# Kernel tuning notes

Measured on AMD Instinct MI355X. Metric: run time of the kernel, lower is better.

## Reference

```python
import jax, jax.numpy as jnp
import numpy as np


def setup_inputs() -> dict:
    key = jax.random.key(0)
    k1, k2, k3 = jax.random.split(key, 3)
    B, C, H, W = 8, 256, 64, 64
    x = jax.random.normal(k1, (B, C, H, W), dtype=jnp.float32)
    mask = (jax.random.uniform(k2, (B, 1, H, W)) < 0.5).astype(jnp.float32)
    # Conv1d(2C, C, kernel_size=1) == matmul with weight (C, 2C) + bias (C,)
    Wc = jax.random.normal(k3, (C, 2 * C), dtype=jnp.float32) * 0.02
    bc = jnp.zeros((C,), dtype=jnp.float32)
    return {"x": x, "mask": mask, "Wc": Wc, "bc": bc}


def reference(x, mask, Wc, bc):
    B, C, H, W = x.shape
    N = H * W
    EPS = 1e-8
    # mask.detach() + nearest interpolate to x's spatial size (sizes already match)
    m = jax.lax.stop_gradient(mask)
    q = (x * m).reshape(B, C, N)              # masked (foreground) features
    s = (x * (1.0 - m)).reshape(B, C, N)      # support (background) features
    q = q / (jnp.linalg.norm(q, axis=1, keepdims=True) + EPS)
    s = s / (jnp.linalg.norm(s, axis=1, keepdims=True) + EPS)
    # per-batch cosine similarity: (B, N, N)
    sim = jnp.einsum('bcn,bcm->bnm', q, s)
    # top-1 over support dim (k = 1)
    idx = jnp.argmax(sim, axis=2)             # (B, N) selected support index per query pos
    wv = jnp.max(sim, axis=2)                 # (B, N) top-1 similarity value
    fore_wv = jnp.max(sim, axis=1)            # (B, N) top-1 over query dim
    fm = m.reshape(B, N)
    # faithful quirk: validmask = validmask[0, :, 0] keeps only support position 0 -> per-sample scalar
    valid = ((fore_wv[:, 0] > 0.5).astype(x.dtype) * fm[:, 0])[:, None, None]  # (B,1,1)
    # gather selected support features: select[b,c,j] = s[b,c,idx[b,j]]
    select = jnp.take_along_axis(s, idx[:, None, :], axis=2)  # (B, C, N)
    # faithful quirk: with k=1, Softmax(dim=-1) acts over the H*W axis (same per channel)
    w = jax.nn.softmax(wv, axis=-1)           # (B, N)
    fuse = select * w[:, None, :]             # (B, C, N)  (sum over k=1 is identity)
    hybrid = jnp.concatenate([fuse, q], axis=1)               # (B, 2C, N)
    hybrid = jnp.einsum('bin,oi->bon', hybrid, Wc) + bc[None, :, None]  # 1x1 conv
    hybrid = hybrid * valid + q * (1.0 - valid)
    refined = hybrid.reshape(B, C, H, W)
    # attmask holds only the LAST sample's indices (loop variable overwritten)
    attmap = jnp.zeros((B, N), dtype=x.dtype).at[:, idx[-1]].set(1.0)
    attmap = attmap.reshape(B, 1, H, W)
    attmap = jnp.repeat(jnp.repeat(attmap, 8, axis=2), 8, axis=3)  # nearest x8 upsample
    out = refined * m + x * (1.0 - m)
    return out, attmap
```

## Files before the change

kernel.cpp:

```cpp
#include <hip/hip_runtime.h>
#include <cmath>

#define B_ 8
#define C_ 256
#define N_ 4096
#define EPS_ 1e-8f

typedef _Float16 half8 __attribute__((ext_vector_type(8)));
typedef float f32x4 __attribute__((ext_vector_type(4)));
typedef unsigned short ushort8 __attribute__((ext_vector_type(8)));

__device__ __forceinline__ void gload_lds16(const void* g, void* l) {
  __builtin_amdgcn_global_load_lds((const __attribute__((address_space(1))) unsigned int*)g,
                                   (__attribute__((address_space(3))) unsigned int*)l, 16, 0, 0);
}

__device__ __forceinline__ float block_fore(const float* __restrict__ partMax, int b) {
  int l = threadIdx.x & 63;
  float v = partMax[(b << 6) + l];
#pragma unroll
  for (int d = 32; d; d >>= 1) v = fmaxf(v, __shfl_xor(v, d, 64));
  return v;
}

__global__ __launch_bounds__(512) void k_base(const float* __restrict__ x, const float* __restrict__ mask,
                                              float* __restrict__ fq, float* __restrict__ fs,
                                              float* __restrict__ out, float* __restrict__ partMax,
                                              int* __restrict__ mark,
                                              unsigned short* __restrict__ qhi, unsigned short* __restrict__ qlo,
                                              unsigned short* __restrict__ shi, unsigned short* __restrict__ slo,
                                              int* __restrict__ rowsrc, int* __restrict__ rowrank,
                                              int* __restrict__ colsrc, int* __restrict__ colmapG,
                                              int* __restrict__ cnt) {
  int b = blockIdx.y, n0 = blockIdx.x << 6;
  int t = threadIdx.x;
  if (b == B_) {
    if (blockIdx.x != 0) return;
    __shared__ int wtot[8], wbase[8], stot_s;
    int n0c = t << 3;
#pragma unroll
    for (int i = 0; i < 8; ++i) {
      rowsrc[t + (i << 9)] = 0;
      colsrc[t + (i << 9)] = 0;
      colmapG[t + (i << 9)] = 0x3fffffff;
    }
    __syncthreads();
    int f[8]; int pk = 0;
#pragma unroll
    for (int i = 0; i < 8; ++i) {
      int m = (mask[(7 << 12) + n0c + i] != 0.f) ? 1 : 0;
      f[i] = m;
      pk += m ? 1 : (1 << 16);
    }
    int incl = pk;
#pragma unroll
    for (int d = 1; d < 64; d <<= 1) {
      int o = __shfl_up(incl, d, 64);
      if ((t & 63) >= d) incl += o;
    }
    if ((t & 63) == 63) wtot[t >> 6] = incl;
    __syncthreads();
    if (t < 8) {
      int s2 = 0;
      for (int i = 0; i < t; ++i) s2 += wtot[i];
      wbase[t] = s2;
      if (t == 7) stot_s = s2 + wtot[7];
    }
    __syncthreads();
    int excl = wbase[t >> 6] + incl - pk;
    int rslot = excl & 0xffff, cslot = excl >> 16;
#pragma unroll
    for (int i = 0; i < 8; ++i) {
      int n2 = n0c + i;
      if (f[i]) { rowsrc[rslot] = n2; rowrank[n2] = rslot; ++rslot; }
      else      { rowrank[n2] = -1; colsrc[cslot] = n2; colmapG[cslot] = n2; ++cslot; }
    }
    __syncthreads();
    if (t == 0) {
      int tot = stot_s;
      int nr = tot & 0xffff;
      cnt[0] = nr;
      cnt[1] = tot >> 16;
      cnt[2] = (nr > 0) ? rowsrc[0] : 0x7fffffff;
    }
    return;
  }
  int ln = t & 63, cg = t >> 6;
  __shared__ float sred[512];
  __shared__ float s0[256];
  __shared__ float rss[8][64], rdp[8][64];
  __shared__ float scaleS[64], f64q[64], f64s[64];
  __shared__ float bcast[2];
  if (b == 0 && blockIdx.x == 0) {
#pragma unroll
    for (int i = 0; i < 8; ++i) mark[t + (i << 9)] = 0;
  }
  const size_t xbase = ((size_t)b * C_) << 12;
  float xc0 = 0.f;
  if (t < 256) xc0 = x[xbase + ((size_t)t << 12)];
  sred[t] = xc0 * xc0;
  __syncthreads();
  for (int s = 256; s; s >>= 1) { if (t < s) sred[t] += sred[t + s]; __syncthreads(); }
  if (t == 0) { bcast[0] = 1.f / (sqrtf(sred[0]) + EPS_); bcast[1] = mask[b << 12]; }
  __syncthreads();
  if (t < 256) s0[t] = xc0 * ((1.f - bcast[1]) * bcast[0]);
  __syncthreads();
  int n = n0 + ln;
  const float* xp = x + xbase + (((size_t)cg) << 17) + n;
  float xv[32];
  float ss = 0.f, dp = 0.f;
#pragma unroll
  for (int c = 0; c < 32; ++c) {
    float v = xp[(size_t)c << 12];
    xv[c] = v;
    ss += v * v;
    dp += v * s0[(cg << 5) + c];
  }
  rss[cg][ln] = ss; rdp[cg][ln] = dp;
  __syncthreads();
  if (t < 64) {
    float sst = 0.f, dpt = 0.f;
#pragma unroll
    for (int g = 0; g < 8; ++g) { sst += rss[g][t]; dpt += rdp[g][t]; }
    float inv = 1.f / (sqrtf(sst) + EPS_);
    float m = mask[(b << 12) + n0 + t];
    float fqv = m * inv;
    fq[(b << 12) + n0 + t] = fqv;
    fs[(b << 12) + n0 + t] = (1.f - m) * inv;
    scaleS[t] = (m != 0.f) ? inv : 1.f;
    f64q[t] = fqv * 64.0f;
    f64s[t] = (1.f - m) * inv * 64.0f;
    float val = dpt * fqv;
#pragma unroll
    for (int d = 32; d; d >>= 1) val = fmaxf(val, __shfl_xor(val, d, 64));
    if (t == 0) partMax[(b << 6) + blockIdx.x] = val;
  }
  __syncthreads();
  float sc = scaleS[ln];
  float* op = out + xbase + (((size_t)cg) << 17) + n;
#pragma unroll
  for (int c = 0; c < 32; ++c) op[(size_t)c << 12] = xv[c] * sc;
  if (b == B_ - 1) {
    float fqn = f64q[ln], fsn = f64s[ln];
    size_t rowbase = ((size_t)n) << 8;
#pragma unroll
    for (int j = 0; j < 4; ++j) {
      ushort8 vqh, vql, vsh, vsl;
#pragma unroll
      for (int i = 0; i < 8; ++i) {
        float xvv = xv[j * 8 + i];
        float qv = xvv * fqn;
        _Float16 qh = (_Float16)qv;
        _Float16 ql = (_Float16)((qv - (float)qh) * 2048.0f);
        float sv = xvv * fsn;
        _Float16 sh = (_Float16)sv;
        _Float16 sl = (_Float16)((sv - (float)sh) * 2048.0f);
        vqh[i] = __builtin_bit_cast(unsigned short, qh);
        vql[i] = __builtin_bit_cast(unsigned short, ql);
        vsh[i] = __builtin_bit_cast(unsigned short, sh);
        vsl[i] = __builtin_bit_cast(unsigned short, sl);
      }
      size_t off = rowbase + ((size_t)cg << 5) + ((size_t)j << 3);
      *reinterpret_cast<ushort8*>(qhi + off) = vqh;
      *reinterpret_cast<ushort8*>(qlo + off) = vql;
      *reinterpret_cast<ushort8*>(shi + off) = vsh;
      *reinterpret_cast<ushort8*>(slo + off) = vsl;
    }
  }
}

__global__ __launch_bounds__(256, 2) void k_sim7(const unsigned short* __restrict__ qhi, const unsigned short* __restrict__ qlo,
                                                 const unsigned short* __restrict__ shi, const unsigned short* __restrict__ slo,
                                                 const int* __restrict__ rowsrc, const int* __restrict__ colsrc,
                                                 const int* __restrict__ colmapG, const int* __restrict__ cnt,
                                                 float* __restrict__ partV, int* __restrict__ partI) {
  int nrows = cnt[0], ncols = cnt[1];
  int bid = blockIdx.x;
  int mt = bid & 31, nt = bid >> 5;
  if ((nt << 7) >= nrows || (mt << 7) >= ncols) return;
  int tid = threadIdx.x;
  int w = tid >> 6, lane = tid & 63;
  int wy = w >> 1, wx = w & 1;
  __shared__ __align__(16) unsigned short smem[2][16384];

  f32x4 acc_h[4][4], acc_c[4][4];
#pragma unroll
  for (int i = 0; i < 4; ++i)
#pragma unroll
    for (int j = 0; j < 4; ++j) {
      acc_h[i][j] = (f32x4){0.f, 0.f, 0.f, 0.f};
      acc_c[i][j] = (f32x4){0.f, 0.f, 0.f, 0.f};
    }

  const unsigned short* gsrc = (w == 0) ? qhi : (w == 1) ? qlo : (w == 2) ? shi : slo;
  const int* srcmap = (w < 2) ? rowsrc : colsrc;
  int n0 = ((w < 2) ? nt : mt) << 7;
  int lrow = lane >> 2, lch = lane & 3;
  int chx = (lch ^ ((lrow >> 1) & 3)) << 3;
  int s = lane >> 4, c16 = lane & 15;
  int srco[8];
#pragma unroll
  for (int seg = 0; seg < 8; ++seg)
    srco[seg] = (srcmap[n0 + (seg << 4) + lrow] << 8) + chx;

#define STAGE7(buf, kt)                                                                \
  _Pragma("unroll")                                                                    \
  for (int seg = 0; seg < 8; ++seg) {                                                  \
    const unsigned short* g = gsrc + (size_t)(srco[seg] + ((kt) << 5));                \
    gload_lds16(g, &smem[buf][(w << 12) + (seg << 9)]);                                \
  }

  STAGE7(0, 0);

  int cur = 0;
  for (int kt = 0; kt < 8; ++kt) {
    if (kt < 7) {
      STAGE7(cur ^ 1, kt + 1);
      asm volatile("s_waitcnt vmcnt(8)" ::: "memory");
    } else {
      asm volatile("s_waitcnt vmcnt(0)" ::: "memory");
    }
    __builtin_amdgcn_s_barrier();
    __builtin_amdgcn_sched_barrier(0);
    const unsigned short* sm = &smem[cur][0];
    half8 ah[4], al[4], bh[4], bl[4];
#pragma unroll
    for (int f = 0; f < 4; ++f) {
      int ra = (wy << 6) + (f << 4) + c16;
      int oa = ra * 32 + ((s ^ ((ra >> 1) & 3)) << 3);
      ah[f] = *reinterpret_cast<const half8*>(&sm[oa]);
      al[f] = *reinterpret_cast<const half8*>(&sm[4096 + oa]);
      int rb = (wx << 6) + (f << 4) + c16;
      int ob = rb * 32 + ((s ^ ((rb >> 1) & 3)) << 3);
      bh[f] = *reinterpret_cast<const half8*>(&sm[8192 + ob]);
      bl[f] = *reinterpret_cast<const half8*>(&sm[12288 + ob]);
    }
#pragma unroll
    for (int fi = 0; fi < 4; ++fi)
#pragma unroll
      for (int fj = 0; fj < 4; ++fj) {
        acc_h[fi][fj] = __builtin_amdgcn_mfma_f32_16x16x32_f16(ah[fi], bh[fj], acc_h[fi][fj], 0, 0, 0);
        acc_c[fi][fj] = __builtin_amdgcn_mfma_f32_16x16x32_f16(ah[fi], bl[fj], acc_c[fi][fj], 0, 0, 0);
        acc_c[fi][fj] = __builtin_amdgcn_mfma_f32_16x16x32_f16(al[fi], bh[fj], acc_c[fi][fj], 0, 0, 0);
      }
    asm volatile("s_waitcnt lgkmcnt(0)" ::: "memory");
    __builtin_amdgcn_s_barrier();
    __builtin_amdgcn_sched_barrier(0);
    cur ^= 1;
  }
#undef STAGE7
  int cg4[4], cok[4];
#pragma unroll
  for (int fj = 0; fj < 4; ++fj) {
    int slotg = (mt << 7) + (wx << 6) + (fj << 4) + c16;
    cg4[fj] = colmapG[slotg];
    cok[fj] = slotg < ncols;
  }
  float* redV = reinterpret_cast<float*>(&smem[0][0]);
  int* redI = reinterpret_cast<int*>(&smem[0][512]);
  int g16 = lane >> 4;
#pragma unroll
  for (int fi = 0; fi < 4; ++fi)
#pragma unroll
    for (int r2 = 0; r2 < 4; ++r2) {
      float bv = -INFINITY; int bi = 0x7fffffff;
#pragma unroll
      for (int fj = 0; fj < 4; ++fj) {
        float v = cok[fj] ? (acc_h[fi][fj][r2] + acc_c[fi][fj][r2] * (1.0f / 2048.0f)) * (1.0f / 4096.0f)
                          : -INFINITY;
        int colg = cg4[fj];
        if (v > bv) { bv = v; bi = colg; }
      }
#pragma unroll
      for (int d = 1; d < 16; d <<= 1) {
        float ov = __shfl_xor(bv, d, 64);
        int oi = __shfl_xor(bi, d, 64);
        if (ov > bv || (ov == bv && oi < bi)) { bv = ov; bi = oi; }
      }
      if (c16 == 0) {
        int row = (wy << 6) + (fi << 4) + (g16 << 2) + r2;
        redV[row * 2 + wx] = bv;
        redI[row * 2 + wx] = bi;
      }
    }
  __syncthreads();
  if (tid < 128) {
    float v0 = redV[tid * 2], v1 = redV[tid * 2 + 1];
    int i0 = redI[tid * 2], i1 = redI[tid * 2 + 1];
    if (v1 > v0 || (v1 == v0 && i1 < i0)) { v0 = v1; i0 = i1; }
    int n = (nt << 7) + tid;
    partV[(((size_t)n) << 5) + mt] = v0;
    partI[(((size_t)n) << 5) + mt] = i0;
  }
}

__global__ __launch_bounds__(256) void k_mid(const float* __restrict__ x, const float* __restrict__ mask,
                                             const float* __restrict__ partMax,
                                             const float* __restrict__ fq, const float* __restrict__ fs,
                                             const float* __restrict__ p7V, const int* __restrict__ p7I,
                                             const int* __restrict__ rowrank, const int* __restrict__ cnt,
                                             float* __restrict__ wv, int* __restrict__ idxv,
                                             int* __restrict__ mark) {
  int bid = blockIdx.x;
  int tid = threadIdx.x;
  if (bid < 16) {
    int n = bid * 256 + tid;
    int ncols = cnt[1], j0 = cnt[2];
    int rk = rowrank[n];
    float bv; int bi;
    if (rk < 0) {
      bv = 0.f; bi = 0;
    } else {
      bv = -INFINITY; bi = 0x7fffffff;
      int mtmax = (ncols + 127) >> 7;
      for (int mt = 0; mt < mtmax; ++mt) {
        float v = p7V[(((size_t)rk) << 5) + mt];
        int i = p7I[(((size_t)rk) << 5) + mt];
        if (v > bv || (v == bv && i < bi)) { bv = v; bi = i; }
      }
      if (j0 < N_) {
        if (0.f > bv) { bv = 0.f; bi = j0; }
        else if (0.f == bv && j0 < bi) bi = j0;
      }
    }
    wv[((B_ - 1) << 12) + n] = bv;
    idxv[((B_ - 1) << 12) + n] = bi;
    mark[bi] = 1;
    return;
  }
  int rr = bid - 16;
  int b = rr >> 6;
  float fore = block_fore(partMax, b);
  if (!(fore > 0.5f) || mask[b << 12] == 0.f) return;
  int n0 = (rr & 63) << 6;
  int tx = tid & 15, ty = tid >> 4;
  int lk = ty, ln4 = tx << 2;

  __shared__ float As[16][68];
  __shared__ float Bs[16][68];
  __shared__ float fqs[64], fss[64];
  __shared__ float rv[64][17];
  __shared__ int ri[64][17];

  if (tid < 64) fqs[tid] = fq[(b << 12) + n0 + tid];

  float bestv[4]; int besti[4];
#pragma unroll
  for (int i = 0; i < 4; ++i) { bestv[i] = -INFINITY; besti[i] = 0; }

  const size_t xb = ((size_t)b * C_) << 12;

  for (int m0 = 0; m0 < N_; m0 += 64) {
    if (tid < 64) fss[tid] = fs[(b << 12) + m0 + tid];
    float cacc[4][4];
#pragma unroll
    for (int i = 0; i < 4; ++i)
#pragma unroll
      for (int j = 0; j < 4; ++j) cacc[i][j] = 0.f;
    __syncthreads();
    for (int kt = 0; kt < C_; kt += 16) {
      float4 va = *reinterpret_cast<const float4*>(x + xb + ((size_t)(kt + lk) << 12) + n0 + ln4);
      float4 vb = *reinterpret_cast<const float4*>(x + xb + ((size_t)(kt + lk) << 12) + m0 + ln4);
      va.x *= fqs[ln4]; va.y *= fqs[ln4 + 1]; va.z *= fqs[ln4 + 2]; va.w *= fqs[ln4 + 3];
      vb.x *= fss[ln4]; vb.y *= fss[ln4 + 1]; vb.z *= fss[ln4 + 2]; vb.w *= fss[ln4 + 3];
      *reinterpret_cast<float4*>(&As[lk][ln4]) = va;
      *reinterpret_cast<float4*>(&Bs[lk][ln4]) = vb;
      __syncthreads();
#pragma unroll
      for (int k = 0; k < 16; ++k) {
        float a0 = As[k][(ty << 2) + 0], a1 = As[k][(ty << 2) + 1], a2 = As[k][(ty << 2) + 2], a3 = As[k][(ty << 2) + 3];
        float b0 = Bs[k][(tx << 2) + 0], b1 = Bs[k][(tx << 2) + 1], b2 = Bs[k][(tx << 2) + 2], b3 = Bs[k][(tx << 2) + 3];
        cacc[0][0] += a0 * b0; cacc[0][1] += a0 * b1; cacc[0][2] += a0 * b2; cacc[0][3] += a0 * b3;
        cacc[1][0] += a1 * b0; cacc[1][1] += a1 * b1; cacc[1][2] += a1 * b2; cacc[1][3] += a1 * b3;
        cacc[2][0] += a2 * b0; cacc[2][1] += a2 * b1; cacc[2][2] += a2 * b2; cacc[2][3] += a2 * b3;
        cacc[3][0] += a3 * b0; cacc[3][1] += a3 * b1; cacc[3][2] += a3 * b2; cacc[3][3] += a3 * b3;
      }
      __syncthreads();
    }
#pragma unroll
    for (int j = 0; j < 4; ++j) {
      int col = m0 + (tx << 2) + j;
#pragma unroll
      for (int i = 0; i < 4; ++i) {
        float v = cacc[i][j];
        if (v > bestv[i]) { bestv[i] = v; besti[i] = col; }
      }
    }
  }
#pragma unroll
  for (int i = 0; i < 4; ++i) { rv[(ty << 2) + i][tx] = bestv[i]; ri[(ty << 2) + i][tx] = besti[i]; }
  __syncthreads();
  if (tid < 64) {
    float bv = rv[tid][0]; int bi = ri[tid][0];
#pragma unroll
    for (int t2 = 1; t2 < 16; ++t2) {
      float v = rv[tid][t2]; int ii = ri[tid][t2];
      if (v > bv || (v == bv && ii < bi)) { bv = v; bi = ii; }
    }
    wv[(b << 12) + n0 + tid] = bv;
    idxv[(b << 12) + n0 + tid] = bi;
  }
}

__global__ __launch_bounds__(256) void k_epi(const int* __restrict__ mark, float* __restrict__ att,
                                             const float* __restrict__ x, const float* __restrict__ mask,
                                             const float* __restrict__ partMax,
                                             const float* __restrict__ fq, const float* __restrict__ fs,
                                             const float* __restrict__ Wc, const float* __restrict__ bc,
                                             const int* __restrict__ idxv, const float* __restrict__ wv,
                                             float* __restrict__ out) {
  int bid = blockIdx.x;
  int tid = threadIdx.x;
  if (bid < 1024) {
    int id = bid * 256 + tid;
    int x8 = (id & 63) << 3;
    int y = (id >> 6) & 511;
    int b = id >> 15;
    float v = mark[((y >> 3) << 6) + (x8 >> 3)] ? 1.f : 0.f;
    float4 vv = make_float4(v, v, v, v);
    float* p = att + (((size_t)b) << 18) + (y << 9) + x8;
    *reinterpret_cast<float4*>(p) = vv;
    *reinterpret_cast<float4*>(p + 4) = vv;
    return;
  }
  int rr = bid - 1024;
  int b = rr >> 4;
  int bx = rr & 15;
  float fore = block_fore(partMax, b);
  if (!(fore > 0.5f) || mask[b << 12] == 0.f) return;
  __shared__ float red[256];
  float mx = -INFINITY;
  for (int n = tid; n < N_; n += 256) mx = fmaxf(mx, wv[(b << 12) + n]);
  red[tid] = mx; __syncthreads();
  for (int s = 128; s; s >>= 1) { if (tid < s) red[tid] = fmaxf(red[tid], red[tid + s]); __syncthreads(); }
  mx = red[0]; __syncthreads();
  float sm = 0.f;
  for (int n = tid; n < N_; n += 256) sm += expf(wv[(b << 12) + n] - mx);
  red[tid] = sm; __syncthreads();
  for (int s = 128; s; s >>= 1) { if (tid < s) red[tid] += red[tid + s]; __syncthreads(); }
  float den = red[0];

  int n = bx * 256 + tid;
  int bn = (b << 12) + n;
  float mn = mask[bn];
  if (mn == 0.f) return;
  int j = idxv[bn];
  float w = expf(wv[bn] - mx) / den;
  float fsj = fs[(b << 12) + j];
  float fqn = fq[bn];
  const float* xb = x + (((size_t)b * C_) << 12);
  for (int o = 0; o < C_; ++o) {
    const float* wr = Wc + o * 2 * C_;
    float a1 = 0.f, a2 = 0.f;
    for (int i = 0; i < C_; ++i) {
      a1 += wr[i] * xb[((size_t)i << 12) + j];
      a2 += wr[C_ + i] * xb[((size_t)i << 12) + n];
    }
    out[((size_t)(b * C_ + o) << 12) + n] = bc[o] + a1 * (fsj * w) + a2 * fqn;
  }
}

extern "C" void kernel_launch(void* const* d_in, const int* in_sizes, int n_in,
                              void* d_out, int out_size, void* d_ws, size_t ws_size,
                              hipStream_t stream) {
  const float* x = (const float*)d_in[0];
  const float* mask = (const float*)d_in[1];
  const float* Wc = (const float*)d_in[2];
  const float* bc = (const float*)d_in[3];
  float* out = (float*)d_out;
  float* att = out + (size_t)B_ * C_ * N_;

  float* wsf = (float*)d_ws;
  float* fq = wsf;
  float* fs = wsf + 32768;
  float* wv = wsf + 65536;
  int* idxv = (int*)(wsf + 98304);
  int* rowsrc = (int*)(wsf + 131072);
  int* rowrank = (int*)(wsf + 135168);
  int* colsrc = (int*)(wsf + 139264);
  int* colmapG = (int*)(wsf + 143360);
  int* cnt = (int*)(wsf + 147456);
  int* mark = (int*)(wsf + 655392);
  float* partMax = wsf + 659488;
  float* p7V = wsf + 660000;
  int* p7I = (int*)(wsf + 791072);
  unsigned short* qhi = (unsigned short*)(wsf + 922144);
  unsigned short* qlo = (unsigned short*)(wsf + 1446432);
  unsigned short* shi = (unsigned short*)(wsf + 1970720);
  unsigned short* slo = (unsigned short*)(wsf + 2495008);

  k_base<<<dim3(64, B_ + 1), 512, 0, stream>>>(x, mask, fq, fs, out, partMax, mark,
                                               qhi, qlo, shi, slo,
                                               rowsrc, rowrank, colsrc, colmapG, cnt);
  k_sim7<<<1024, 256, 0, stream>>>(qhi, qlo, shi, slo, rowsrc, colsrc, colmapG, cnt, p7V, p7I);
  k_mid<<<464, 256, 0, stream>>>(x, mask, partMax, fq, fs, p7V, p7I, rowrank, cnt, wv, idxv, mark);
  k_epi<<<1152, 256, 0, stream>>>(mark, att, x, mask, partMax, fq, fs, Wc, bc, idxv, wv, out);
}
```

Baseline: 62.40 us.

## Fuse sim7 and mid kernels with last-block atomic reduction and 8-wave tiles

```diff
diff --git a/kernel.cpp b/kernel.cpp
--- a/kernel.cpp
+++ b/kernel.cpp
@@ -82,6 +82,7 @@
       cnt[0] = nr;
       cnt[1] = tot >> 16;
       cnt[2] = (nr > 0) ? rowsrc[0] : 0x7fffffff;
+      cnt[4] = 0;
     }
     return;
   }
@@ -169,178 +170,200 @@
   }
 }
 
-__global__ __launch_bounds__(256, 2) void k_sim7(const unsigned short* __restrict__ qhi, const unsigned short* __restrict__ qlo,
+__global__ __launch_bounds__(512, 2) void k_sim7(const unsigned short* __restrict__ qhi, const unsigned short* __restrict__ qlo,
                                                  const unsigned short* __restrict__ shi, const unsigned short* __restrict__ slo,
-                                                 const int* __restrict__ rowsrc, const int* __restrict__ colsrc,
-                                                 const int* __restrict__ colmapG, const int* __restrict__ cnt,
-                                                 float* __restrict__ partV, int* __restrict__ partI) {
-  int nrows = cnt[0], ncols = cnt[1];
-  int bid = blockIdx.x;
-  int mt = bid & 31, nt = bid >> 5;
-  if ((nt << 7) >= nrows || (mt << 7) >= ncols) return;
-  int tid = threadIdx.x;
-  int w = tid >> 6, lane = tid & 63;
-  int wy = w >> 1, wx = w & 1;
+                                                 const int* __restrict__ rowsrc, const int* __restrict__ rowrank,
+                                                 const int* __restrict__ colsrc, const int* __restrict__ colmapG,
+                                                 int* __restrict__ cnt,
+                                                 float* __restrict__ partV, int* __restrict__ partI,
+                                                 const float* __restrict__ x, const float* __restrict__ mask,
+                                                 const float* __restrict__ partMax,
+                                                 const float* __restrict__ fq, const float* __restrict__ fs,
+                                                 float* __restrict__ wv, int* __restrict__ idxv,
+                                                 int* __restrict__ mark) {
   __shared__ __align__(16) unsigned short smem[2][16384];
-
-  f32x4 acc_h[4][4], acc_c[4][4];
-#pragma unroll
-  for (int i = 0; i < 4; ++i)
-#pragma unroll
-    for (int j = 0; j < 4; ++j) {
-      acc_h[i][j] = (f32x4){0.f, 0.f, 0.f, 0.f};
-      acc_c[i][j] = (f32x4){0.f, 0.f, 0.f, 0.f};
-    }
-
-  const unsigned short* gsrc = (w == 0) ? qhi : (w == 1) ? qlo : (w == 2) ? shi : slo;
-  const int* srcmap = (w < 2) ? rowsrc : colsrc;
-  int n0 = ((w < 2) ? nt : mt) << 7;
-  int lrow = lane >> 2, lch = lane & 3;
-  int chx = (lch ^ ((lrow >> 1) & 3)) << 3;
-  int s = lane >> 4, c16 = lane & 15;
-  int srco[8];
-#pragma unroll
-  for (int seg = 0; seg < 8; ++seg)
-    srco[seg] = (srcmap[n0 + (seg << 4) + lrow] << 8) + chx;
-
-#define STAGE7(buf, kt)                                                                \
-  _Pragma("unroll")                                                                    \
-  for (int seg = 0; seg < 8; ++seg) {                                                  \
-    const unsigned short* g = gsrc + (size_t)(srco[seg] + ((kt) << 5));                \
-    gload_lds16(g, &smem[buf][(w << 12) + (seg << 9)]);                                \
-  }
-
-  STAGE7(0, 0);
-
-  int cur = 0;
-  for (int kt = 0; kt < 8; ++kt) {
-    if (kt < 7) {
-      STAGE7(cur ^ 1, kt + 1);
-      asm volatile("s_waitcnt vmcnt(8)" ::: "memory");
-    } else {
-      asm volatile("s_waitcnt vmcnt(0)" ::: "memory");
-    }
-    __builtin_amdgcn_s_barrier();
-    __builtin_amdgcn_sched_barrier(0);
-    const unsigned short* sm = &smem[cur][0];
-    half8 ah[4], al[4], bh[4], bl[4];
-#pragma unroll
-    for (int f = 0; f < 4; ++f) {
-      int ra = (wy << 6) + (f << 4) + c16;
-      int oa = ra * 32 + ((s ^ ((ra >> 1) & 3)) << 3);
-      ah[f] = *reinterpret_cast<const half8*>(&sm[oa]);
-      al[f] = *reinterpret_cast<const half8*>(&sm[4096 + oa]);
-      int rb = (wx << 6) + (f << 4) + c16;
-      int ob = rb * 32 + ((s ^ ((rb >> 1) & 3)) << 3);
-      bh[f] = *reinterpret_cast<const half8*>(&sm[8192 + ob]);
-      bl[f] = *reinterpret_cast<const half8*>(&sm[12288 + ob]);
-    }
-#pragma unroll
-    for (int fi = 0; fi < 4; ++fi)
-#pragma unroll
-      for (int fj = 0; fj < 4; ++fj) {
-        acc_h[fi][fj] = __builtin_amdgcn_mfma_f32_16x16x32_f16(ah[fi], bh[fj], acc_h[fi][fj], 0, 0, 0);
-        acc_c[fi][fj] = __builtin_amdgcn_mfma_f32_16x16x32_f16(ah[fi], bl[fj], acc_c[fi][fj], 0, 0, 0);
-        acc_c[fi][fj] = __builtin_amdgcn_mfma_f32_16x16x32_f16(al[fi], bh[fj], acc_c[fi][fj], 0, 0, 0);
-      }
-    asm volatile("s_waitcnt lgkmcnt(0)" ::: "memory");
-    __builtin_amdgcn_s_barrier();
-    __builtin_amdgcn_sched_barrier(0);
-    cur ^= 1;
-  }
-#undef STAGE7
-  int cg4[4], cok[4];
-#pragma unroll
-  for (int fj = 0; fj < 4; ++fj) {
-    int slotg = (mt << 7) + (wx << 6) + (fj << 4) + c16;
-    cg4[fj] = colmapG[slotg];
-    cok[fj] = slotg < ncols;
-  }
-  float* redV = reinterpret_cast<float*>(&smem[0][0]);
-  int* redI = reinterpret_cast<int*>(&smem[0][512]);
-  int g16 = lane >> 4;
-#pragma unroll
-  for (int fi = 0; fi < 4; ++fi)
-#pragma unroll
-    for (int r2 = 0; r2 < 4; ++r2) {
-      float bv = -INFINITY; int bi = 0x7fffffff;
-#pragma unroll
-      for (int fj = 0; fj < 4; ++fj) {
-        float v = cok[fj] ? (acc_h[fi][fj][r2] + acc_c[fi][fj][r2] * (1.0f / 2048.0f)) * (1.0f / 4096.0f)
-                          : -INFINITY;
-        int colg = cg4[fj];
-        if (v > bv) { bv = v; bi = colg; }
-      }
-#pragma unroll
-      for (int d = 1; d < 16; d <<= 1) {
-        float ov = __shfl_xor(bv, d, 64);
-        int oi = __shfl_xor(bi, d, 64);
-        if (ov > bv || (ov == bv && oi < bi)) { bv = ov; bi = oi; }
-      }
-      if (c16 == 0) {
-        int row = (wy << 6) + (fi << 4) + (g16 << 2) + r2;
-        redV[row * 2 + wx] = bv;
-        redI[row * 2 + wx] = bi;
-      }
-    }
-  __syncthreads();
-  if (tid < 128) {
-    float v0 = redV[tid * 2], v1 = redV[tid * 2 + 1];
-    int i0 = redI[tid * 2], i1 = redI[tid * 2 + 1];
-    if (v1 > v0 || (v1 == v0 && i1 < i0)) { v0 = v1; i0 = i1; }
-    int n = (nt << 7) + tid;
-    partV[(((size_t)n) << 5) + mt] = v0;
-    partI[(((size_t)n) << 5) + mt] = i0;
-  }
-}
-
-__global__ __launch_bounds__(256) void k_mid(const float* __restrict__ x, const float* __restrict__ mask,
-                                             const float* __restrict__ partMax,
-                                             const float* __restrict__ fq, const float* __restrict__ fs,
-                                             const float* __restrict__ p7V, const int* __restrict__ p7I,
-                                             const int* __restrict__ rowrank, const int* __restrict__ cnt,
-                                             float* __restrict__ wv, int* __restrict__ idxv,
-                                             int* __restrict__ mark) {
+  __shared__ int lastblk;
   int bid = blockIdx.x;
   int tid = threadIdx.x;
-  if (bid < 16) {
-    int n = bid * 256 + tid;
-    int ncols = cnt[1], j0 = cnt[2];
-    int rk = rowrank[n];
-    float bv; int bi;
-    if (rk < 0) {
-      bv = 0.f; bi = 0;
-    } else {
-      bv = -INFINITY; bi = 0x7fffffff;
-      int mtmax = (ncols + 127) >> 7;
-      for (int mt = 0; mt < mtmax; ++mt) {
-        float v = p7V[(((size_t)rk) << 5) + mt];
-        int i = p7I[(((size_t)rk) << 5) + mt];
-        if (v > bv || (v == bv && i < bi)) { bv = v; bi = i; }
-      }
-      if (j0 < N_) {
-        if (0.f > bv) { bv = 0.f; bi = j0; }
-        else if (0.f == bv && j0 < bi) bi = j0;
-      }
-    }
-    wv[((B_ - 1) << 12) + n] = bv;
-    idxv[((B_ - 1) << 12) + n] = bi;
-    mark[bi] = 1;
+
+  if (bid < 1024) {
+    int nrows = cnt[0], ncols = cnt[1];
+    int mt = bid & 31, nt = bid >> 5;
+    int active = !(((nt << 7) >= nrows) || ((mt << 7) >= ncols));
+    if (active) {
+      int w = tid >> 6, lane = tid & 63;
+      int wy = w >> 2, wx = w & 3;
+      int arr = w >> 1, shalf = w & 1;
+
+      f32x4 acc_h[4][2], acc_c[4][2];
+#pragma unroll
+      for (int i = 0; i < 4; ++i)
+#pragma unroll
+        for (int j = 0; j < 2; ++j) {
+          acc_h[i][j] = (f32x4){0.f, 0.f, 0.f, 0.f};
+          acc_c[i][j] = (f32x4){0.f, 0.f, 0.f, 0.f};
+        }
+
+      const unsigned short* gsrc = (arr == 0) ? qhi : (arr == 1) ? qlo : (arr == 2) ? shi : slo;
+      const int* srcmap = (arr < 2) ? rowsrc : colsrc;
+      int n0 = ((arr < 2) ? nt : mt) << 7;
+      int lrow = lane >> 2, lch = lane & 3;
+      int chx = (lch ^ ((lrow >> 1) & 3)) << 3;
+      int s = lane >> 4, c16 = lane & 15;
+      int srco[4];
+#pragma unroll
+      for (int s2 = 0; s2 < 4; ++s2) {
+        int seg = (shalf << 2) + s2;
+        srco[s2] = (srcmap[n0 + (seg << 4) + lrow] << 8) + chx;
+      }
+
+#define STAGE7(buf, kt)                                                                   \
+  _Pragma("unroll")                                                                       \
+  for (int s2 = 0; s2 < 4; ++s2) {                                                        \
+    const unsigned short* g = gsrc + (size_t)(srco[s2] + ((kt) << 5));                    \
+    gload_lds16(g, &smem[buf][(arr << 12) + ((((shalf << 2) + s2)) << 9)]);               \
+  }
+
+      STAGE7(0, 0);
+
+      int cur = 0;
+      for (int kt = 0; kt < 8; ++kt) {
+        if (kt < 7) {
+          STAGE7(cur ^ 1, kt + 1);
+          asm volatile("s_waitcnt vmcnt(4)" ::: "memory");
+        } else {
+          asm volatile("s_waitcnt vmcnt(0)" ::: "memory");
+        }
+        __builtin_amdgcn_s_barrier();
+        __builtin_amdgcn_sched_barrier(0);
+        const unsigned short* sm = &smem[cur][0];
+        half8 ah[4], al[4], bh[2], bl[2];
+#pragma unroll
+        for (int f = 0; f < 4; ++f) {
+          int ra = (wy << 6) + (f << 4) + c16;
+          int oa = ra * 32 + ((s ^ ((ra >> 1) & 3)) << 3);
+          ah[f] = *reinterpret_cast<const half8*>(&sm[oa]);
+          al[f] = *reinterpret_cast<const half8*>(&sm[4096 + oa]);
+        }
+#pragma unroll
+        for (int f = 0; f < 2; ++f) {
+          int rb = (wx << 5) + (f << 4) + c16;
+          int ob = rb * 32 + ((s ^ ((rb >> 1) & 3)) << 3);
+          bh[f] = *reinterpret_cast<const half8*>(&sm[8192 + ob]);
+          bl[f] = *reinterpret_cast<const half8*>(&sm[12288 + ob]);
+        }
+#pragma unroll
+        for (int fi = 0; fi < 4; ++fi)
+#pragma unroll
+          for (int fj = 0; fj < 2; ++fj) {
+            acc_h[fi][fj] = __builtin_amdgcn_mfma_f32_16x16x32_f16(ah[fi], bh[fj], acc_h[fi][fj], 0, 0, 0);
+            acc_c[fi][fj] = __builtin_amdgcn_mfma_f32_16x16x32_f16(ah[fi], bl[fj], acc_c[fi][fj], 0, 0, 0);
+            acc_c[fi][fj] = __builtin_amdgcn_mfma_f32_16x16x32_f16(al[fi], bh[fj], acc_c[fi][fj], 0, 0, 0);
+          }
+        asm volatile("s_waitcnt lgkmcnt(0)" ::: "memory");
+        __builtin_amdgcn_s_barrier();
+        __builtin_amdgcn_sched_barrier(0);
+        cur ^= 1;
+      }
+#undef STAGE7
+      int cg4[2], cok[2];
+#pragma unroll
+      for (int fj = 0; fj < 2; ++fj) {
+        int slotg = (mt << 7) + (wx << 5) + (fj << 4) + c16;
+        cg4[fj] = colmapG[slotg];
+        cok[fj] = slotg < ncols;
+      }
+      float* redV = reinterpret_cast<float*>(&smem[0][0]);
+      int* redI = reinterpret_cast<int*>(&smem[0][1024]);
+      int g16 = lane >> 4;
+#pragma unroll
+      for (int fi = 0; fi < 4; ++fi)
+#pragma unroll
+        for (int r2 = 0; r2 < 4; ++r2) {
+          float bv = -INFINITY; int bi = 0x7fffffff;
+#pragma unroll
+          for (int fj = 0; fj < 2; ++fj) {
+            float v = cok[fj] ? (acc_h[fi][fj][r2] + acc_c[fi][fj][r2] * (1.0f / 2048.0f)) * (1.0f / 4096.0f)
+                              : -INFINITY;
+            int colg = cg4[fj];
+            if (v > bv) { bv = v; bi = colg; }
+          }
+#pragma unroll
+          for (int d = 1; d < 16; d <<= 1) {
+            float ov = __shfl_xor(bv, d, 64);
+            int oi = __shfl_xor(bi, d, 64);
+            if (ov > bv || (ov == bv && oi < bi)) { bv = ov; bi = oi; }
+          }
+          if (c16 == 0) {
+            int row = (wy << 6) + (fi << 4) + (g16 << 2) + r2;
+            redV[row * 4 + wx] = bv;
+            redI[row * 4 + wx] = bi;
+          }
+        }
+      __syncthreads();
+      if (tid < 128) {
+        float bv = redV[tid * 4]; int bi = redI[tid * 4];
+#pragma unroll
+        for (int q = 1; q < 4; ++q) {
+          float v = redV[tid * 4 + q]; int i = redI[tid * 4 + q];
+          if (v > bv || (v == bv && i < bi)) { bv = v; bi = i; }
+        }
+        int n = (nt << 7) + tid;
+        partV[(((size_t)n) << 5) + mt] = bv;
+        partI[(((size_t)n) << 5) + mt] = bi;
+      }
+    }
+    __threadfence();
+    if (tid == 0) {
+      int old = atomicAdd(&cnt[4], 1);
+      lastblk = (old == 1023) ? 1 : 0;
+    }
+    __syncthreads();
+    if (lastblk) {
+      __threadfence();
+      int ncols2 = cnt[1], j0 = cnt[2];
+      int mtmax = (ncols2 + 127) >> 7;
+#pragma unroll
+      for (int rr2 = 0; rr2 < 8; ++rr2) {
+        int n = (rr2 << 9) + tid;
+        int rk = rowrank[n];
+        float bv; int bi;
+        if (rk < 0) {
+          bv = 0.f; bi = 0;
+        } else {
+          bv = -INFINITY; bi = 0x7fffffff;
+          for (int mt2 = 0; mt2 < mtmax; ++mt2) {
+            float v = partV[(((size_t)rk) << 5) + mt2];
+            int i = partI[(((size_t)rk) << 5) + mt2];
+            if (v > bv || (v == bv && i < bi)) { bv = v; bi = i; }
+          }
+          if (j0 < N_) {
+            if (0.f > bv) { bv = 0.f; bi = j0; }
+            else if (0.f == bv && j0 < bi) bi = j0;
+          }
+        }
+        wv[((B_ - 1) << 12) + n] = bv;
+        idxv[((B_ - 1) << 12) + n] = bi;
+        mark[bi] = 1;
+      }
+    }
     return;
   }
-  int rr = bid - 16;
+
+  int rr = bid - 1024;
   int b = rr >> 6;
   float fore = block_fore(partMax, b);
   if (!(fore > 0.5f) || mask[b << 12] == 0.f) return;
+  if (tid >= 256) return;
   int n0 = (rr & 63) << 6;
   int tx = tid & 15, ty = tid >> 4;
   int lk = ty, ln4 = tx << 2;
-
-  __shared__ float As[16][68];
-  __shared__ float Bs[16][68];
-  __shared__ float fqs[64], fss[64];
-  __shared__ float rv[64][17];
-  __shared__ int ri[64][17];
+  float* As = reinterpret_cast<float*>(&smem[0][0]);
+  float* Bs = As + 1088;
+  float* fqs = Bs + 1088;
+  float* fss = fqs + 64;
+  float* rv = fss + 64;
+  int* ri = reinterpret_cast<int*>(rv + 1088);
 
   if (tid < 64) fqs[tid] = fq[(b << 12) + n0 + tid];
 
@@ -363,13 +386,15 @@
       float4 vb = *reinterpret_cast<const float4*>(x + xb + ((size_t)(kt + lk) << 12) + m0 + ln4);
       va.x *= fqs[ln4]; va.y *= fqs[ln4 + 1]; va.z *= fqs[ln4 + 2]; va.w *= fqs[ln4 + 3];
       vb.x *= fss[ln4]; vb.y *= fss[ln4 + 1]; vb.z *= fss[ln4 + 2]; vb.w *= fss[ln4 + 3];
-      *reinterpret_cast<float4*>(&As[lk][ln4]) = va;
-      *reinterpret_cast<float4*>(&Bs[lk][ln4]) = vb;
+      *reinterpret_cast<float4*>(&As[lk * 68 + ln4]) = va;
+      *reinterpret_cast<float4*>(&Bs[lk * 68 + ln4]) = vb;
       __syncthreads();
 #pragma unroll
       for (int k = 0; k < 16; ++k) {
-        float a0 = As[k][(ty << 2) + 0], a1 = As[k][(ty << 2) + 1], a2 = As[k][(ty << 2) + 2], a3 = As[k][(ty << 2) + 3];
-        float b0 = Bs[k][(tx << 2) + 0], b1 = Bs[k][(tx << 2) + 1], b2 = Bs[k][(tx << 2) + 2], b3 = Bs[k][(tx << 2) + 3];
+        float a0 = As[k * 68 + (ty << 2) + 0], a1 = As[k * 68 + (ty << 2) + 1];
+        float a2 = As[k * 68 + (ty << 2) + 2], a3 = As[k * 68 + (ty << 2) + 3];
+        float b0 = Bs[k * 68 + (tx << 2) + 0], b1 = Bs[k * 68 + (tx << 2) + 1];
+        float b2 = Bs[k * 68 + (tx << 2) + 2], b3 = Bs[k * 68 + (tx << 2) + 3];
         cacc[0][0] += a0 * b0; cacc[0][1] += a0 * b1; cacc[0][2] += a0 * b2; cacc[0][3] += a0 * b3;
         cacc[1][0] += a1 * b0; cacc[1][1] += a1 * b1; cacc[1][2] += a1 * b2; cacc[1][3] += a1 * b3;
         cacc[2][0] += a2 * b0; cacc[2][1] += a2 * b1; cacc[2][2] += a2 * b2; cacc[2][3] += a2 * b3;
@@ -388,13 +413,13 @@
     }
   }
 #pragma unroll
-  for (int i = 0; i < 4; ++i) { rv[(ty << 2) + i][tx] = bestv[i]; ri[(ty << 2) + i][tx] = besti[i]; }
+  for (int i = 0; i < 4; ++i) { rv[((ty << 2) + i) * 17 + tx] = bestv[i]; ri[((ty << 2) + i) * 17 + tx] = besti[i]; }
   __syncthreads();
   if (tid < 64) {
-    float bv = rv[tid][0]; int bi = ri[tid][0];
+    float bv = rv[tid * 17]; int bi = ri[tid * 17];
 #pragma unroll
     for (int t2 = 1; t2 < 16; ++t2) {
-      float v = rv[tid][t2]; int ii = ri[tid][t2];
+      float v = rv[tid * 17 + t2]; int ii = ri[tid * 17 + t2];
       if (v > bv || (v == bv && ii < bi)) { bv = v; bi = ii; }
     }
     wv[(b << 12) + n0 + tid] = bv;
@@ -492,7 +517,7 @@
   k_base<<<dim3(64, B_ + 1), 512, 0, stream>>>(x, mask, fq, fs, out, partMax, mark,
                                                qhi, qlo, shi, slo,
                                                rowsrc, rowrank, colsrc, colmapG, cnt);
-  k_sim7<<<1024, 256, 0, stream>>>(qhi, qlo, shi, slo, rowsrc, colsrc, colmapG, cnt, p7V, p7I);
-  k_mid<<<464, 256, 0, stream>>>(x, mask, partMax, fq, fs, p7V, p7I, rowrank, cnt, wv, idxv, mark);
+  k_sim7<<<1472, 512, 0, stream>>>(qhi, qlo, shi, slo, rowsrc, rowrank, colsrc, colmapG, cnt,
+                                   p7V, p7I, x, mask, partMax, fq, fs, wv, idxv, mark);
   k_epi<<<1152, 256, 0, stream>>>(mark, att, x, mask, partMax, fq, fs, Wc, bc, idxv, wv, out);
 }
```

Measured after the change: 242.0 us. +287.8%, slower.

## Split k_sim7 128x128 tile across eight waves instead of four

Applied to the files above, without the earlier changes.

```diff
diff --git a/kernel.cpp b/kernel.cpp
--- a/kernel.cpp
+++ b/kernel.cpp
@@ -169,7 +169,7 @@
   }
 }
 
-__global__ __launch_bounds__(256, 2) void k_sim7(const unsigned short* __restrict__ qhi, const unsigned short* __restrict__ qlo,
+__global__ __launch_bounds__(512, 2) void k_sim7(const unsigned short* __restrict__ qhi, const unsigned short* __restrict__ qlo,
                                                  const unsigned short* __restrict__ shi, const unsigned short* __restrict__ slo,
                                                  const int* __restrict__ rowsrc, const int* __restrict__ colsrc,
                                                  const int* __restrict__ colmapG, const int* __restrict__ cnt,
@@ -180,34 +180,37 @@
   if ((nt << 7) >= nrows || (mt << 7) >= ncols) return;
   int tid = threadIdx.x;
   int w = tid >> 6, lane = tid & 63;
-  int wy = w >> 1, wx = w & 1;
+  int wy = w >> 2, wx = w & 3;
+  int arr = w >> 1, shalf = w & 1;
   __shared__ __align__(16) unsigned short smem[2][16384];
 
-  f32x4 acc_h[4][4], acc_c[4][4];
+  f32x4 acc_h[4][2], acc_c[4][2];
 #pragma unroll
   for (int i = 0; i < 4; ++i)
 #pragma unroll
-    for (int j = 0; j < 4; ++j) {
+    for (int j = 0; j < 2; ++j) {
       acc_h[i][j] = (f32x4){0.f, 0.f, 0.f, 0.f};
       acc_c[i][j] = (f32x4){0.f, 0.f, 0.f, 0.f};
     }
 
-  const unsigned short* gsrc = (w == 0) ? qhi : (w == 1) ? qlo : (w == 2) ? shi : slo;
-  const int* srcmap = (w < 2) ? rowsrc : colsrc;
-  int n0 = ((w < 2) ? nt : mt) << 7;
+  const unsigned short* gsrc = (arr == 0) ? qhi : (arr == 1) ? qlo : (arr == 2) ? shi : slo;
+  const int* srcmap = (arr < 2) ? rowsrc : colsrc;
+  int n0 = ((arr < 2) ? nt : mt) << 7;
   int lrow = lane >> 2, lch = lane & 3;
   int chx = (lch ^ ((lrow >> 1) & 3)) << 3;
   int s = lane >> 4, c16 = lane & 15;
-  int srco[8];
-#pragma unroll
-  for (int seg = 0; seg < 8; ++seg)
-    srco[seg] = (srcmap[n0 + (seg << 4) + lrow] << 8) + chx;
-
-#define STAGE7(buf, kt)                                                                \
-  _Pragma("unroll")                                                                    \
-  for (int seg = 0; seg < 8; ++seg) {                                                  \
-    const unsigned short* g = gsrc + (size_t)(srco[seg] + ((kt) << 5));                \
-    gload_lds16(g, &smem[buf][(w << 12) + (seg << 9)]);                                \
+  int srco[4];
+#pragma unroll
+  for (int s2 = 0; s2 < 4; ++s2) {
+    int seg = (shalf << 2) + s2;
+    srco[s2] = (srcmap[n0 + (seg << 4) + lrow] << 8) + chx;
+  }
+
+#define STAGE7(buf, kt)                                                                   \
+  _Pragma("unroll")                                                                       \
+  for (int s2 = 0; s2 < 4; ++s2) {                                                        \
+    const unsigned short* g = gsrc + (size_t)(srco[s2] + ((kt) << 5));                    \
+    gload_lds16(g, &smem[buf][(arr << 12) + ((((shalf << 2) + s2)) << 9)]);               \
   }
 
   STAGE7(0, 0);
@@ -216,21 +219,24 @@
   for (int kt = 0; kt < 8; ++kt) {
     if (kt < 7) {
       STAGE7(cur ^ 1, kt + 1);
-      asm volatile("s_waitcnt vmcnt(8)" ::: "memory");
+      asm volatile("s_waitcnt vmcnt(4)" ::: "memory");
     } else {
       asm volatile("s_waitcnt vmcnt(0)" ::: "memory");
     }
     __builtin_amdgcn_s_barrier();
     __builtin_amdgcn_sched_barrier(0);
     const unsigned short* sm = &smem[cur][0];
-    half8 ah[4], al[4], bh[4], bl[4];
+    half8 ah[4], al[4], bh[2], bl[2];
 #pragma unroll
     for (int f = 0; f < 4; ++f) {
       int ra = (wy << 6) + (f << 4) + c16;
       int oa = ra * 32 + ((s ^ ((ra >> 1) & 3)) << 3);
       ah[f] = *reinterpret_cast<const half8*>(&sm[oa]);
       al[f] = *reinterpret_cast<const half8*>(&sm[4096 + oa]);
-      int rb = (wx << 6) + (f << 4) + c16;
+    }
+#pragma unroll
+    for (int f = 0; f < 2; ++f) {
+      int rb = (wx << 5) + (f << 4) + c16;
       int ob = rb * 32 + ((s ^ ((rb >> 1) & 3)) << 3);
       bh[f] = *reinterpret_cast<const half8*>(&sm[8192 + ob]);
       bl[f] = *reinterpret_cast<const half8*>(&sm[12288 + ob]);
@@ -238,7 +244,7 @@
 #pragma unroll
     for (int fi = 0; fi < 4; ++fi)
 #pragma unroll
-      for (int fj = 0; fj < 4; ++fj) {
+      for (int fj = 0; fj < 2; ++fj) {
         acc_h[fi][fj] = __builtin_amdgcn_mfma_f32_16x16x32_f16(ah[fi], bh[fj], acc_h[fi][fj], 0, 0, 0);
         acc_c[fi][fj] = __builtin_amdgcn_mfma_f32_16x16x32_f16(ah[fi], bl[fj], acc_c[fi][fj], 0, 0, 0);
         acc_c[fi][fj] = __builtin_amdgcn_mfma_f32_16x16x32_f16(al[fi], bh[fj], acc_c[fi][fj], 0, 0, 0);
@@ -249,15 +255,15 @@
     cur ^= 1;
   }
 #undef STAGE7
-  int cg4[4], cok[4];
-#pragma unroll
-  for (int fj = 0; fj < 4; ++fj) {
-    int slotg = (mt << 7) + (wx << 6) + (fj << 4) + c16;
+  int cg4[2], cok[2];
+#pragma unroll
+  for (int fj = 0; fj < 2; ++fj) {
+    int slotg = (mt << 7) + (wx << 5) + (fj << 4) + c16;
     cg4[fj] = colmapG[slotg];
     cok[fj] = slotg < ncols;
   }
   float* redV = reinterpret_cast<float*>(&smem[0][0]);
-  int* redI = reinterpret_cast<int*>(&smem[0][512]);
+  int* redI = reinterpret_cast<int*>(&smem[0][1024]);
   int g16 = lane >> 4;
 #pragma unroll
   for (int fi = 0; fi < 4; ++fi)
@@ -265,7 +271,7 @@
     for (int r2 = 0; r2 < 4; ++r2) {
       float bv = -INFINITY; int bi = 0x7fffffff;
 #pragma unroll
-      for (int fj = 0; fj < 4; ++fj) {
+      for (int fj = 0; fj < 2; ++fj) {
         float v = cok[fj] ? (acc_h[fi][fj][r2] + acc_c[fi][fj][r2] * (1.0f / 2048.0f)) * (1.0f / 4096.0f)
                           : -INFINITY;
         int colg = cg4[fj];
@@ -279,18 +285,21 @@
       }
       if (c16 == 0) {
         int row = (wy << 6) + (fi << 4) + (g16 << 2) + r2;
-        redV[row * 2 + wx] = bv;
-        redI[row * 2 + wx] = bi;
+        redV[row * 4 + wx] = bv;
+        redI[row * 4 + wx] = bi;
       }
     }
   __syncthreads();
   if (tid < 128) {
-    float v0 = redV[tid * 2], v1 = redV[tid * 2 + 1];
-    int i0 = redI[tid * 2], i1 = redI[tid * 2 + 1];
-    if (v1 > v0 || (v1 == v0 && i1 < i0)) { v0 = v1; i0 = i1; }
+    float bv = redV[tid * 4]; int bi = redI[tid * 4];
+#pragma unroll
+    for (int q = 1; q < 4; ++q) {
+      float v = redV[tid * 4 + q]; int i = redI[tid * 4 + q];
+      if (v > bv || (v == bv && i < bi)) { bv = v; bi = i; }
+    }
     int n = (nt << 7) + tid;
-    partV[(((size_t)n) << 5) + mt] = v0;
-    partI[(((size_t)n) << 5) + mt] = i0;
+    partV[(((size_t)n) << 5) + mt] = bv;
+    partI[(((size_t)n) << 5) + mt] = bi;
   }
 }
 
@@ -492,7 +501,7 @@
   k_base<<<dim3(64, B_ + 1), 512, 0, stream>>>(x, mask, fq, fs, out, partMax, mark,
                                                qhi, qlo, shi, slo,
                                                rowsrc, rowrank, colsrc, colmapG, cnt);
-  k_sim7<<<1024, 256, 0, stream>>>(qhi, qlo, shi, slo, rowsrc, colsrc, colmapG, cnt, p7V, p7I);
+  k_sim7<<<1024, 512, 0, stream>>>(qhi, qlo, shi, slo, rowsrc, colsrc, colmapG, cnt, p7V, p7I);
   k_mid<<<464, 256, 0, stream>>>(x, mask, partMax, fq, fs, p7V, p7I, rowrank, cnt, wv, idxv, mark);
   k_epi<<<1152, 256, 0, stream>>>(mark, att, x, mask, partMax, fq, fs, Wc, bc, idxv, wv, out);
 }
```

Result: no change. 62.12 us (-0.4%).
